# Optimization experiments

Hardware: AMD Instinct MI355X
Metric: run time of the kernel (lower is better)

The kernel has to match this reference:

```python
import jax, jax.numpy as jnp
import numpy as np

D_MODEL = 1024
N_HEADS = 16
ADAPTIVE_TEMP = 1.0
LN_EPS = 1e-5


def _sinusoidal_pe(max_len, d_model):
    pos = np.arange(max_len)[:, None].astype(np.float32)
    div = np.exp(np.arange(0, d_model, 2).astype(np.float32) * (-np.log(10000.0) / d_model))
    pe = np.zeros((max_len, d_model), dtype=np.float32)
    pe[:, 0::2] = np.sin(pos * div)
    pe[:, 1::2] = np.cos(pos * div)
    return jnp.asarray(pe)


def _mlp2(q, w1, b1, w2, b2):
    # Linear(1,h) -> ReLU -> Linear(h,d)
    return jax.nn.relu(q @ w1 + b1) @ w2 + b2


def setup_inputs() -> dict:
    key = jax.random.key(0)
    ks = jax.random.split(key, 24)
    B, T, D = 2, 2048, D_MODEL
    H2 = D // 2
    s = 0.02
    inp = {
        "x": jax.random.normal(ks[0], (B, T, D), jnp.float32),
        "quantile": jax.random.uniform(ks[1], (B, 1), jnp.float32),
        "quantile_importance": jax.random.uniform(ks[2], (100,), jnp.float32),
        "Wq": jax.random.normal(ks[3], (D, D), jnp.float32) * s,
        "bq": jnp.zeros((D,), jnp.float32),
        "Wk": jax.random.normal(ks[4], (D, D), jnp.float32) * s,
        "bk": jnp.zeros((D,), jnp.float32),
        "Wv": jax.random.normal(ks[5], (D, D), jnp.float32) * s,
        "bv": jnp.zeros((D,), jnp.float32),
        "Wo": jax.random.normal(ks[6], (D, D), jnp.float32) * s,
        "bo": jnp.zeros((D,), jnp.float32),
        "qpq_w1": jax.random.normal(ks[7], (1, H2), jnp.float32) * s,
        "qpq_b1": jnp.zeros((H2,), jnp.float32),
        "qpq_w2": jax.random.normal(ks[8], (H2, D), jnp.float32) * s,
        "qpq_b2": jnp.zeros((D,), jnp.float32),
        "qpk_w1": jax.random.normal(ks[9], (1, H2), jnp.float32) * s,
        "qpk_b1": jnp.zeros((H2,), jnp.float32),
        "qpk_w2": jax.random.normal(ks[10], (H2, D), jnp.float32) * s,
        "qpk_b2": jnp.zeros((D,), jnp.float32),
        "qpv_w1": jax.random.normal(ks[11], (1, H2), jnp.float32) * s,
        "qpv_b1": jnp.zeros((H2,), jnp.float32),
        "qpv_w2": jax.random.normal(ks[12], (H2, D), jnp.float32) * s,
        "qpv_b2": jnp.zeros((D,), jnp.float32),
        "ln_g": jnp.ones((D,), jnp.float32),
        "ln_b": jnp.zeros((D,), jnp.float32),
    }
    return inp


def reference(x, quantile, quantile_importance,
              Wq, bq, Wk, bk, Wv, bv, Wo, bo,
              qpq_w1, qpq_b1, qpq_w2, qpq_b2,
              qpk_w1, qpk_b1, qpk_w2, qpk_b2,
              qpv_w1, qpv_b1, qpv_w2, qpv_b2,
              ln_g, ln_b):
    B, T, D = x.shape
    H = N_HEADS
    dk = D // H

    # positional encoding
    x = x + _sinusoidal_pe(T, D)

    # quantile-conditioned embeddings [B, D]
    q_embed = _mlp2(quantile, qpq_w1, qpq_b1, qpq_w2, qpq_b2)
    k_embed = _mlp2(quantile, qpk_w1, qpk_b1, qpk_w2, qpk_b2)
    v_embed = _mlp2(quantile, qpv_w1, qpv_b1, qpv_w2, qpv_b2)

    # importance weight per batch (no-grad buffer lookup)
    buf = jax.lax.stop_gradient(quantile_importance)
    idx = jnp.clip((quantile[:, 0] * 100).astype(jnp.int32), 0, 99)
    mx = buf.max()
    imp = buf[idx]
    imp = jnp.where(mx > 0, imp / mx, imp)  # [B]

    Q = (x @ Wq + bq) + q_embed[:, None, :]
    K = (x @ Wk + bk) + k_embed[:, None, :]
    V = (x @ Wv + bv) + v_embed[:, None, :]

    # [B, H, T, dk]
    Q = Q.reshape(B, T, H, dk).transpose(0, 2, 1, 3)
    K = K.reshape(B, T, H, dk).transpose(0, 2, 1, 3)
    V = V.reshape(B, T, H, dk).transpose(0, 2, 1, 3)

    scores = jnp.einsum('bhtd,bhsd->bhts', Q, K) / jnp.sqrt(jnp.float32(dk))
    scale = 1.0 + imp * ADAPTIVE_TEMP  # [B]
    scores = scores * scale[:, None, None, None]

    attn = jax.nn.softmax(scores, axis=-1)  # dropout is identity at inference
    out = jnp.einsum('bhts,bhsd->bhtd', attn, V)
    out = out.transpose(0, 2, 1, 3).reshape(B, T, D)
    out = out @ Wo + bo

    y = x + out
    mu = y.mean(axis=-1, keepdims=True)
    var = y.var(axis=-1, keepdims=True)
    return (y - mu) / jnp.sqrt(var + LN_EPS) * ln_g + ln_b
```

## Files before the change

kernel.cpp:

```cpp
#include <hip/hip_runtime.h>

#define D 1024
#define T 2048
#define BATCH 2
#define NR 4096
#define NH 16
#define HID 512

typedef unsigned short u16;
typedef unsigned int u32;
typedef unsigned long long u64;
typedef float f32x4 __attribute__((ext_vector_type(4)));
typedef float f32x16 __attribute__((ext_vector_type(16)));
typedef __bf16 bf16x8 __attribute__((ext_vector_type(8)));

__device__ __forceinline__ u16 f2bf(float f) {
    union { __bf16 h; u16 u; } c; c.h = (__bf16)f; return c.u;
}

__device__ __forceinline__ u32 cvtpk(float a, float b) {
    u32 r;
    asm("v_cvt_pk_bf16_f32 %0, %1, %2" : "=v"(r) : "v"(a), "v"(b));
    return r;
}

__device__ __forceinline__ void plswap(u32& x, u32& y) {
    asm volatile("v_permlane32_swap_b32 %0, %1" : "+v"(x), "+v"(y));
}

__device__ __forceinline__ void gload16(const u16* g, u16* l) {
    __builtin_amdgcn_global_load_lds(
        (const __attribute__((address_space(1))) unsigned int*)g,
        (__attribute__((address_space(3))) unsigned int*)l,
        16, 0, 0);
}

__global__ __launch_bounds__(256) void k_mlp1(const float* __restrict__ qtl,
        const float* __restrict__ w1q, const float* __restrict__ b1q, const float* __restrict__ w2q,
        const float* __restrict__ w1k, const float* __restrict__ b1k, const float* __restrict__ w2k,
        const float* __restrict__ w1v, const float* __restrict__ b1v, const float* __restrict__ w2v,
        const float* __restrict__ qimp, float* __restrict__ part, float* __restrict__ scl)
{
    int dc = blockIdx.x;
    int jc = blockIdx.y;
    int wb = blockIdx.z;
    int which = wb >> 1, b = wb & 1;
    const float *w1, *b1, *w2;
    if (which == 0)      { w1 = w1q; b1 = b1q; w2 = w2q; }
    else if (which == 1) { w1 = w1k; b1 = b1k; w2 = w2k; }
    else                 { w1 = w1v; b1 = b1v; w2 = w2v; }
    int tid = threadIdx.x;
    __shared__ float h[128];
    if (tid < 128) {
        int j = jc * 128 + tid;
        h[tid] = fmaxf(qtl[b] * w1[j] + b1[j], 0.0f);
    }
    __syncthreads();
    int d = dc * 256 + tid;
    float acc = 0.0f;
    for (int j = 0; j < 128; ++j) acc += h[j] * w2[(size_t)(jc * 128 + j) * D + d];
    part[((size_t)wb * 4 + jc) * D + d] = acc;
    if (dc == 0 && jc == 0 && wb == 0 && tid < BATCH) {
        float mx = qimp[0];
        for (int i = 1; i < 100; ++i) mx = fmaxf(mx, qimp[i]);
        float q = qtl[tid];
        int idx = (int)(q * 100.0f);
        idx = idx < 0 ? 0 : (idx > 99 ? 99 : idx);
        float imp = qimp[idx];
        if (mx > 0.0f) imp /= mx;
        scl[tid] = 1.0f + imp;
    }
}

__global__ __launch_bounds__(256) void k_mlp2(const float* __restrict__ part,
        const float* __restrict__ b2q, const float* __restrict__ b2k, const float* __restrict__ b2v,
        float* __restrict__ embeds)
{
    int dc = blockIdx.x;
    int wb = blockIdx.y;
    int which = wb >> 1;
    const float* b2 = which == 0 ? b2q : which == 1 ? b2k : b2v;
    int d = dc * 256 + threadIdx.x;
    float acc = b2[d];
    #pragma unroll
    for (int jc = 0; jc < 4; ++jc) acc += part[((size_t)wb * 4 + jc) * D + d];
    embeds[(size_t)wb * D + d] = acc;
}

__global__ __launch_bounds__(256) void k_pe(const float* __restrict__ x,
                                            float* __restrict__ xpe, u16* __restrict__ xpeb)
{
    int idx = (blockIdx.x * 256 + threadIdx.x) * 4;
    int d = idx & (D - 1);
    int t = (idx >> 10) & (T - 1);
    const float KL = -0.0089944731946f;
    float ft = (float)t;
    float dv0 = __expf((float)d * KL);
    float dv1 = __expf((float)(d + 2) * KL);
    float a0 = ft * dv0, a1 = ft * dv1;
    float4 xv = *reinterpret_cast<const float4*>(x + idx);
    float4 r;
    r.x = xv.x + __sinf(a0);
    r.y = xv.y + __cosf(a0);
    r.z = xv.z + __sinf(a1);
    r.w = xv.w + __cosf(a1);
    *reinterpret_cast<float4*>(xpe + idx) = r;
    ushort4 o;
    o.x = f2bf(r.x); o.y = f2bf(r.y); o.z = f2bf(r.z); o.w = f2bf(r.w);
    *reinterpret_cast<ushort4*>(xpeb + idx) = o;
}

__global__ __launch_bounds__(256) void k_wconv(const float* __restrict__ Wq, const float* __restrict__ Wk,
                                               const float* __restrict__ Wv, const float* __restrict__ Wo,
                                               u16* __restrict__ Wt)
{
    __shared__ float tile[64][65];
    int z = blockIdx.z;
    const float* W = z == 0 ? Wq : z == 1 ? Wk : z == 2 ? Wv : Wo;
    u16* out = Wt + (size_t)z * D * D;
    int n0 = blockIdx.x * 64, k0 = blockIdx.y * 64;
    int r = threadIdx.x >> 4;
    int c4 = (threadIdx.x & 15) * 4;
    #pragma unroll
    for (int rr = 0; rr < 64; rr += 16) {
        float4 v = *reinterpret_cast<const float4*>(W + (size_t)(k0 + r + rr) * D + n0 + c4);
        tile[r + rr][c4 + 0] = v.x; tile[r + rr][c4 + 1] = v.y;
        tile[r + rr][c4 + 2] = v.z; tile[r + rr][c4 + 3] = v.w;
    }
    __syncthreads();
    #pragma unroll
    for (int rr = 0; rr < 64; rr += 16) {
        ushort4 o;
        o.x = f2bf(tile[c4 + 0][r + rr]);
        o.y = f2bf(tile[c4 + 1][r + rr]);
        o.z = f2bf(tile[c4 + 2][r + rr]);
        o.w = f2bf(tile[c4 + 3][r + rr]);
        *reinterpret_cast<ushort4*>(out + (size_t)(n0 + r + rr) * D + k0 + c4) = o;
    }
}

__device__ __forceinline__ void gemm128(const u16* __restrict__ Ag, const u16* __restrict__ Bg,
                                        int m0, int n0, f32x4 acc[4][4])
{
    __shared__ u16 As[128 * 64];
    __shared__ u16 Bs[128 * 64];
    const int tid = threadIdx.x;
    const int lane = tid & 63, wave = tid >> 6;
    const int wr = wave >> 1, wc = wave & 1;
    #pragma unroll
    for (int i = 0; i < 4; ++i)
        #pragma unroll
        for (int j = 0; j < 4; ++j)
            #pragma unroll
            for (int e = 0; e < 4; ++e) acc[i][j][e] = 0.0f;

    for (int kt = 0; kt < 16; ++kt) {
        __syncthreads();
        #pragma unroll
        for (int c = 0; c < 4; ++c) {
            int ci = c * 256 + tid;
            int row = ci >> 3;
            int sl = (ci & 7) ^ (row & 7);
            gload16(Ag + (size_t)(m0 + row) * D + kt * 64 + sl * 8, As + (size_t)ci * 8);
            gload16(Bg + (size_t)(n0 + row) * D + kt * 64 + sl * 8, Bs + (size_t)ci * 8);
        }
        __syncthreads();
        #pragma unroll
        for (int ks = 0; ks < 2; ++ks) {
            bf16x8 af[4], bfr[4];
            #pragma unroll
            for (int i = 0; i < 4; ++i) {
                int ra = wr * 64 + i * 16 + (lane & 15);
                int sa = ((ks * 4 + (lane >> 4)) ^ (ra & 7));
                af[i] = *reinterpret_cast<const bf16x8*>((const char*)As + ra * 128 + sa * 16);
                int rb = wc * 64 + i * 16 + (lane & 15);
                int sb = ((ks * 4 + (lane >> 4)) ^ (rb & 7));
                bfr[i] = *reinterpret_cast<const bf16x8*>((const char*)Bs + rb * 128 + sb * 16);
            }
            #pragma unroll
            for (int i = 0; i < 4; ++i)
                #pragma unroll
                for (int j = 0; j < 4; ++j)
                    acc[i][j] = __builtin_amdgcn_mfma_f32_16x16x32_bf16(af[i], bfr[j], acc[i][j], 0, 0, 0);
        }
    }
}

__global__ __launch_bounds__(256, 2)
void k_qkv(const u16* __restrict__ A, const u16* __restrict__ Wt,
           const float* __restrict__ bq, const float* __restrict__ bk, const float* __restrict__ bv,
           const float* __restrict__ embeds, const float* __restrict__ scl,
           u16* __restrict__ Qo, u16* __restrict__ Ko, u16* __restrict__ Vt)
{
    int which = blockIdx.z;
    const u16* Bg = Wt + (size_t)which * D * D;
    const float* bias = which == 0 ? bq : which == 1 ? bk : bv;
    const float* emb = embeds + which * (BATCH * D);
    int m0 = blockIdx.x * 128, n0 = blockIdx.y * 128;
    f32x4 acc[4][4];
    gemm128(A, Bg, m0, n0, acc);
    int lane = threadIdx.x & 63, wave = threadIdx.x >> 6;
    int wr = wave >> 1, wc = wave & 1;
    int rowbase = m0 + wr * 64 + ((lane >> 4) << 2);
    int colbase = n0 + wc * 64 + (lane & 15);
    if (which < 2) {
        u16* Out = which == 0 ? Qo : Ko;
        float sc0 = 1.0f, sc1 = 1.0f;
        if (which == 0) {
            sc0 = scl[0] * 0.125f * 1.44269504f;
            sc1 = scl[1] * 0.125f * 1.44269504f;
        }
        #pragma unroll
        for (int j = 0; j < 4; ++j) {
            int c = colbase + j * 16;
            float add0 = bias[c] + emb[c];
            float add1 = bias[c] + emb[D + c];
            #pragma unroll
            for (int i = 0; i < 4; ++i) {
                int rb = rowbase + i * 16;
                #pragma unroll
                for (int jj = 0; jj < 4; ++jj) {
                    int r = rb + jj;
                    float v = (r >> 11) ? (acc[i][j][jj] + add1) * sc1
                                        : (acc[i][j][jj] + add0) * sc0;
                    Out[(size_t)r * D + c] = f2bf(v);
                }
            }
        }
    } else {
        #pragma unroll
        for (int j = 0; j < 4; ++j) {
            int c = colbase + j * 16;
            int hh = c >> 6, cc = c & 63;
            float add0 = bias[c] + emb[c];
            float add1 = bias[c] + emb[D + c];
            #pragma unroll
            for (int i = 0; i < 4; ++i) {
                int rb = rowbase + i * 16;
                int bb = rb >> 11;
                int t = rb & (T - 1);
                float add = bb ? add1 : add0;
                ushort4 o;
                o.x = f2bf(acc[i][j][0] + add);
                o.y = f2bf(acc[i][j][1] + add);
                o.z = f2bf(acc[i][j][2] + add);
                o.w = f2bf(acc[i][j][3] + add);
                *reinterpret_cast<ushort4*>(Vt + ((size_t)((bb * NH + hh) * 64 + cc)) * T + t) = o;
            }
        }
    }
}

__global__ __launch_bounds__(256, 2)
void k_attn(const u16* __restrict__ Q, const u16* __restrict__ K, const u16* __restrict__ Vt,
            u16* __restrict__ AO)
{
    __shared__ u16 Ks[2][128 * 64];
    __shared__ u16 Vs[2][64 * 128];
    int bh = blockIdx.x;
    int b = bh >> 4, hh = bh & 15;
    int q0 = blockIdx.y * 128;
    int tid = threadIdx.x;
    int lane = tid & 63, w = tid >> 6;
    int q31 = lane & 31, h = lane >> 5;

    bf16x8 qf[4];
    {
        const u16* qp = Q + (size_t)(b * T + q0 + w * 32 + q31) * D + hh * 64 + h * 8;
        #pragma unroll
        for (int ds = 0; ds < 4; ++ds)
            qf[ds] = *reinterpret_cast<const bf16x8*>(qp + ds * 16);
    }

    f32x16 o0, o1;
    #pragma unroll
    for (int e = 0; e < 16; ++e) { o0[e] = 0.0f; o1[e] = 0.0f; }
    float m_run = -1e30f, l_run = 0.0f;

    #pragma unroll
    for (int c = 0; c < 4; ++c) {
        int ci = c * 256 + tid;
        int row = ci >> 3;
        int sl = (ci & 7) ^ (row & 7);
        gload16(K + (size_t)(b * T + row) * D + hh * 64 + sl * 8, Ks[0] + (size_t)ci * 8);
        int rv = ci >> 4;
        int sv = (ci & 15) ^ (rv & 7);
        gload16(Vt + (size_t)(bh * 64 + rv) * T + sv * 8, Vs[0] + (size_t)ci * 8);
    }
    __syncthreads();

    for (int kt = 0; kt < 16; ++kt) {
        int cur = kt & 1;
        if (kt < 15) {
            int t0 = (kt + 1) * 128;
            #pragma unroll
            for (int c = 0; c < 4; ++c) {
                int ci = c * 256 + tid;
                int row = ci >> 3;
                int sl = (ci & 7) ^ (row & 7);
                gload16(K + (size_t)(b * T + t0 + row) * D + hh * 64 + sl * 8, Ks[cur ^ 1] + (size_t)ci * 8);
                int rv = ci >> 4;
                int sv = (ci & 15) ^ (rv & 7);
                gload16(Vt + (size_t)(bh * 64 + rv) * T + t0 + sv * 8, Vs[cur ^ 1] + (size_t)ci * 8);
            }
        }
        const char* Ksc = (const char*)Ks[cur];
        const char* Vsc = (const char*)Vs[cur];

        f32x16 s[4];
        #pragma unroll
        for (int k2 = 0; k2 < 4; ++k2)
            #pragma unroll
            for (int e = 0; e < 16; ++e) s[k2][e] = 0.0f;
        __builtin_amdgcn_s_setprio(1);
        #pragma unroll
        for (int k2 = 0; k2 < 4; ++k2) {
            int rk = k2 * 32 + q31;
            int xm = rk & 7;
            #pragma unroll
            for (int ds = 0; ds < 4; ++ds) {
                int sp = (2 * ds + h) ^ xm;
                bf16x8 kf = *reinterpret_cast<const bf16x8*>(Ksc + rk * 128 + sp * 16);
                s[k2] = __builtin_amdgcn_mfma_f32_32x32x16_bf16(kf, qf[ds], s[k2], 0, 0, 0);
            }
        }
        __builtin_amdgcn_s_setprio(0);

        float mt = -1e30f;
        #pragma unroll
        for (int k2 = 0; k2 < 4; ++k2)
            #pragma unroll
            for (int e = 0; e < 16; ++e) mt = fmaxf(mt, s[k2][e]);
        mt = fmaxf(mt, __shfl_xor(mt, 32, 64));
        bool skip = __all((int)(mt <= m_run + 11.0f));
        if (!skip) {
            float mn = fmaxf(m_run, mt);
            float corr = __builtin_exp2f(m_run - mn);
            m_run = mn;
            l_run *= corr;
            #pragma unroll
            for (int reg = 0; reg < 16; ++reg) {
                int src = ((reg & 3) + 8 * (reg >> 2)) + ((lane & 32) >> 3);
                float cr = __shfl(corr, src, 64);
                o0[reg] *= cr;
                o1[reg] *= cr;
            }
        }
        float ps0 = 0.0f, ps1 = 0.0f;
        #pragma unroll
        for (int k2 = 0; k2 < 4; ++k2)
            #pragma unroll
            for (int e = 0; e < 16; ++e) {
                float p = __builtin_exp2f(s[k2][e] - m_run);
                s[k2][e] = p;
                if (k2 & 1) ps1 += p; else ps0 += p;
            }
        float psum = ps0 + ps1;
        psum += __shfl_xor(psum, 32, 64);
        l_run += psum;

        __builtin_amdgcn_s_setprio(1);
        #pragma unroll
        for (int k2 = 0; k2 < 4; ++k2) {
            u32 w0 = cvtpk(s[k2][0], s[k2][1]),   w1 = cvtpk(s[k2][2], s[k2][3]);
            u32 w2 = cvtpk(s[k2][4], s[k2][5]),   w3 = cvtpk(s[k2][6], s[k2][7]);
            u32 w4 = cvtpk(s[k2][8], s[k2][9]),   w5 = cvtpk(s[k2][10], s[k2][11]);
            u32 w6 = cvtpk(s[k2][12], s[k2][13]), w7 = cvtpk(s[k2][14], s[k2][15]);
            plswap(w0, w2); plswap(w1, w3);
            plswap(w4, w6); plswap(w5, w7);
            union { bf16x8 v; u32 u[4]; } plo, phi;
            plo.u[0] = w0; plo.u[1] = w1; plo.u[2] = w2; plo.u[3] = w3;
            phi.u[0] = w4; phi.u[1] = w5; phi.u[2] = w6; phi.u[3] = w7;
            int rv0 = q31, rv1 = 32 + q31;
            int x0 = rv0 & 7, x1 = rv1 & 7;
            int klo = 2 * k2, khi = 2 * k2 + 1;
            bf16x8 vf;
            vf = *reinterpret_cast<const bf16x8*>(Vsc + rv0 * 256 + (((2 * klo + h) ^ x0) << 4));
            o0 = __builtin_amdgcn_mfma_f32_32x32x16_bf16(plo.v, vf, o0, 0, 0, 0);
            vf = *reinterpret_cast<const bf16x8*>(Vsc + rv1 * 256 + (((2 * klo + h) ^ x1) << 4));
            o1 = __builtin_amdgcn_mfma_f32_32x32x16_bf16(plo.v, vf, o1, 0, 0, 0);
            vf = *reinterpret_cast<const bf16x8*>(Vsc + rv0 * 256 + (((2 * khi + h) ^ x0) << 4));
            o0 = __builtin_amdgcn_mfma_f32_32x32x16_bf16(phi.v, vf, o0, 0, 0, 0);
            vf = *reinterpret_cast<const bf16x8*>(Vsc + rv1 * 256 + (((2 * khi + h) ^ x1) << 4));
            o1 = __builtin_amdgcn_mfma_f32_32x32x16_bf16(phi.v, vf, o1, 0, 0, 0);
        }
        __builtin_amdgcn_s_setprio(0);
        __syncthreads();
    }

    float linv = 1.0f / l_run;
    #pragma unroll
    for (int reg = 0; reg < 16; ++reg) {
        int src = ((reg & 3) + 8 * (reg >> 2)) + ((lane & 32) >> 3);
        float li = __shfl(linv, src, 64);
        int qr = q0 + w * 32 + (reg & 3) + 8 * (reg >> 2) + 4 * h;
        size_t off = (size_t)(b * T + qr) * D + hh * 64 + q31;
        AO[off] = f2bf(o0[reg] * li);
        AO[off + 32] = f2bf(o1[reg] * li);
    }
}

__global__ __launch_bounds__(256, 2)
void k_ogemm(const u16* __restrict__ A, const u16* __restrict__ Wt,
             const float* __restrict__ bo, const float* __restrict__ xpe,
             float* __restrict__ y)
{
    int m0 = blockIdx.x * 128, n0 = blockIdx.y * 128;
    f32x4 acc[4][4];
    gemm128(A, Wt, m0, n0, acc);
    int lane = threadIdx.x & 63, wave = threadIdx.x >> 6;
    int wr = wave >> 1, wc = wave & 1;
    int rowbase = m0 + wr * 64 + ((lane >> 4) << 2);
    int colbase = n0 + wc * 64 + (lane & 15);
    #pragma unroll
    for (int j = 0; j < 4; ++j) {
        int c = colbase + j * 16;
        float bc = bo[c];
        #pragma unroll
        for (int i = 0; i < 4; ++i) {
            #pragma unroll
            for (int jj = 0; jj < 4; ++jj) {
                int r = rowbase + i * 16 + jj;
                y[(size_t)r * D + c] = acc[i][j][jj] + bc + xpe[(size_t)r * D + c];
            }
        }
    }
}

__global__ __launch_bounds__(256) void k_ln(const float* __restrict__ y, const float* __restrict__ g,
                                            const float* __restrict__ bb, float* __restrict__ out)
{
    int row = blockIdx.x;
    int tid = threadIdx.x;
    const float* yr = y + (size_t)row * D;
    float4 v = *reinterpret_cast<const float4*>(yr + tid * 4);
    float s = v.x + v.y + v.z + v.w;
    float s2 = v.x * v.x + v.y * v.y + v.z * v.z + v.w * v.w;
    #pragma unroll
    for (int off = 1; off < 64; off <<= 1) {
        s += __shfl_xor(s, off, 64);
        s2 += __shfl_xor(s2, off, 64);
    }
    __shared__ float red[8];
    int wave = tid >> 6, lane = tid & 63;
    if (lane == 0) { red[wave] = s; red[4 + wave] = s2; }
    __syncthreads();
    s = red[0] + red[1] + red[2] + red[3];
    s2 = red[4] + red[5] + red[6] + red[7];
    float mu = s * (1.0f / 1024.0f);
    float var = s2 * (1.0f / 1024.0f) - mu * mu;
    float rstd = rsqrtf(var + 1e-5f);
    float4 gv = *reinterpret_cast<const float4*>(g + tid * 4);
    float4 bv = *reinterpret_cast<const float4*>(bb + tid * 4);
    float4 o;
    o.x = (v.x - mu) * rstd * gv.x + bv.x;
    o.y = (v.y - mu) * rstd * gv.y + bv.y;
    o.z = (v.z - mu) * rstd * gv.z + bv.z;
    o.w = (v.w - mu) * rstd * gv.w + bv.w;
    *reinterpret_cast<float4*>(out + (size_t)row * D + tid * 4) = o;
}

extern "C" void kernel_launch(void* const* d_in, const int* in_sizes, int n_in,
                              void* d_out, int out_size, void* d_ws, size_t ws_size,
                              hipStream_t stream)
{
    const float* x    = (const float*)d_in[0];
    const float* qtl  = (const float*)d_in[1];
    const float* qimp = (const float*)d_in[2];
    const float* Wq = (const float*)d_in[3];
    const float* bq = (const float*)d_in[4];
    const float* Wk = (const float*)d_in[5];
    const float* bk = (const float*)d_in[6];
    const float* Wv = (const float*)d_in[7];
    const float* bv = (const float*)d_in[8];
    const float* Wo = (const float*)d_in[9];
    const float* bo = (const float*)d_in[10];
    const float* qpq_w1 = (const float*)d_in[11];
    const float* qpq_b1 = (const float*)d_in[12];
    const float* qpq_w2 = (const float*)d_in[13];
    const float* qpq_b2 = (const float*)d_in[14];
    const float* qpk_w1 = (const float*)d_in[15];
    const float* qpk_b1 = (const float*)d_in[16];
    const float* qpk_w2 = (const float*)d_in[17];
    const float* qpk_b2 = (const float*)d_in[18];
    const float* qpv_w1 = (const float*)d_in[19];
    const float* qpv_b1 = (const float*)d_in[20];
    const float* qpv_w2 = (const float*)d_in[21];
    const float* qpv_b2 = (const float*)d_in[22];
    const float* ln_g = (const float*)d_in[23];
    const float* ln_b = (const float*)d_in[24];
    (void)in_sizes; (void)n_in; (void)out_size; (void)ws_size;

    char* w = (char*)d_ws;
    float* xpe   = (float*)(w);
    u16* xpeb    = (u16*)(w + (16u << 20));
    u16* Wt      = (u16*)(w + (24u << 20));
    u16* Qb      = (u16*)(w + (32u << 20));
    u16* Kb      = (u16*)(w + (40u << 20));
    u16* Vtb     = (u16*)(w + (48u << 20));
    u16* AOb     = (u16*)(w + (56u << 20));
    float* yb    = (float*)(w + (32u << 20));
    float* emb   = (float*)(w + (64u << 20));
    float* scl   = (float*)(w + (64u << 20) + 32768);
    float* part  = (float*)(w + (64u << 20) + 65536);

    k_mlp1<<<dim3(4, 4, 6), 256, 0, stream>>>(qtl,
        qpq_w1, qpq_b1, qpq_w2,
        qpk_w1, qpk_b1, qpk_w2,
        qpv_w1, qpv_b1, qpv_w2,
        qimp, part, scl);
    k_mlp2<<<dim3(4, 6), 256, 0, stream>>>(part, qpq_b2, qpk_b2, qpv_b2, emb);
    k_pe<<<4096, 256, 0, stream>>>(x, xpe, xpeb);
    k_wconv<<<dim3(16, 16, 4), 256, 0, stream>>>(Wq, Wk, Wv, Wo, Wt);
    k_qkv<<<dim3(32, 8, 3), 256, 0, stream>>>(xpeb, Wt, bq, bk, bv, emb, scl, Qb, Kb, Vtb);
    k_attn<<<dim3(32, 16), 256, 0, stream>>>(Qb, Kb, Vtb, AOb);
    k_ogemm<<<dim3(32, 8), 256, 0, stream>>>(AOb, Wt + (size_t)3 * D * D, bo, xpe, yb);
    k_ln<<<4096, 256, 0, stream>>>(yb, ln_g, ln_b, (float*)d_out);
}
```

Before: 162.4 us.

## Split attention KV range across two wave groups per block with LDS merge

```diff
diff --git a/kernel.cpp b/kernel.cpp
--- a/kernel.cpp
+++ b/kernel.cpp
@@ -28,11 +28,30 @@
     asm volatile("v_permlane32_swap_b32 %0, %1" : "+v"(x), "+v"(y));
 }
 
+__device__ __forceinline__ float fmax3(float a, float b, float c) {
+    float r; asm("v_max3_f32 %0, %1, %2, %3" : "=v"(r) : "v"(a), "v"(b), "v"(c)); return r;
+}
+
+__device__ __forceinline__ float vmax16(const f32x16& v) {
+    float c0 = fmax3(v[0], v[1], v[2]);
+    float c1 = fmax3(v[3], v[4], v[5]);
+    float c2 = fmax3(v[6], v[7], v[8]);
+    float c3 = fmax3(v[9], v[10], v[11]);
+    c0 = fmax3(c0, v[12], v[13]);
+    c1 = fmax3(c1, v[14], v[15]);
+    c0 = fmax3(c0, c1, c2);
+    return fmaxf(c0, c3);
+}
+
 __device__ __forceinline__ void gload16(const u16* g, u16* l) {
     __builtin_amdgcn_global_load_lds(
         (const __attribute__((address_space(1))) unsigned int*)g,
         (__attribute__((address_space(3))) unsigned int*)l,
         16, 0, 0);
+}
+
+__device__ __forceinline__ int swz8(int row) {
+    return (row & 7) ^ ((row >> 3) & 3);
 }
 
 __global__ __launch_bounds__(256) void k_mlp1(const float* __restrict__ qtl,
@@ -251,22 +270,25 @@
     }
 }
 
-__global__ __launch_bounds__(256, 2)
+__global__ __launch_bounds__(512, 4)
 void k_attn(const u16* __restrict__ Q, const u16* __restrict__ K, const u16* __restrict__ Vt,
             u16* __restrict__ AO)
 {
-    __shared__ u16 Ks[2][128 * 64];
-    __shared__ u16 Vs[2][64 * 128];
+    __shared__ u16 Ks[2][2][64 * 64];
+    __shared__ u16 Vs[2][2][64 * 64];
     int bh = blockIdx.x;
     int b = bh >> 4, hh = bh & 15;
     int q0 = blockIdx.y * 128;
     int tid = threadIdx.x;
     int lane = tid & 63, w = tid >> 6;
+    int half = w >> 2, wq = w & 3;
     int q31 = lane & 31, h = lane >> 5;
+    int sh = tid >> 8, sti = tid & 255;
+    int kvb = sh * 1024;
 
     bf16x8 qf[4];
     {
-        const u16* qp = Q + (size_t)(b * T + q0 + w * 32 + q31) * D + hh * 64 + h * 8;
+        const u16* qp = Q + (size_t)(b * T + q0 + wq * 32 + q31) * D + hh * 64 + h * 8;
         #pragma unroll
         for (int ds = 0; ds < 4; ++ds)
             qf[ds] = *reinterpret_cast<const bf16x8*>(qp + ds * 16);
@@ -278,45 +300,41 @@
     float m_run = -1e30f, l_run = 0.0f;
 
     #pragma unroll
-    for (int c = 0; c < 4; ++c) {
-        int ci = c * 256 + tid;
+    for (int c = 0; c < 2; ++c) {
+        int ci = c * 256 + sti;
         int row = ci >> 3;
-        int sl = (ci & 7) ^ (row & 7);
-        gload16(K + (size_t)(b * T + row) * D + hh * 64 + sl * 8, Ks[0] + (size_t)ci * 8);
-        int rv = ci >> 4;
-        int sv = (ci & 15) ^ (rv & 7);
-        gload16(Vt + (size_t)(bh * 64 + rv) * T + sv * 8, Vs[0] + (size_t)ci * 8);
+        int sl = (ci & 7) ^ swz8(row);
+        gload16(K + (size_t)(b * T + kvb + row) * D + hh * 64 + sl * 8, Ks[sh][0] + (size_t)ci * 8);
+        gload16(Vt + (size_t)(bh * 64 + row) * T + kvb + sl * 8, Vs[sh][0] + (size_t)ci * 8);
     }
     __syncthreads();
 
     for (int kt = 0; kt < 16; ++kt) {
         int cur = kt & 1;
         if (kt < 15) {
-            int t0 = (kt + 1) * 128;
-            #pragma unroll
-            for (int c = 0; c < 4; ++c) {
-                int ci = c * 256 + tid;
+            int t0 = kvb + (kt + 1) * 64;
+            #pragma unroll
+            for (int c = 0; c < 2; ++c) {
+                int ci = c * 256 + sti;
                 int row = ci >> 3;
-                int sl = (ci & 7) ^ (row & 7);
-                gload16(K + (size_t)(b * T + t0 + row) * D + hh * 64 + sl * 8, Ks[cur ^ 1] + (size_t)ci * 8);
-                int rv = ci >> 4;
-                int sv = (ci & 15) ^ (rv & 7);
-                gload16(Vt + (size_t)(bh * 64 + rv) * T + t0 + sv * 8, Vs[cur ^ 1] + (size_t)ci * 8);
-            }
-        }
-        const char* Ksc = (const char*)Ks[cur];
-        const char* Vsc = (const char*)Vs[cur];
-
-        f32x16 s[4];
-        #pragma unroll
-        for (int k2 = 0; k2 < 4; ++k2)
+                int sl = (ci & 7) ^ swz8(row);
+                gload16(K + (size_t)(b * T + t0 + row) * D + hh * 64 + sl * 8, Ks[sh][cur ^ 1] + (size_t)ci * 8);
+                gload16(Vt + (size_t)(bh * 64 + row) * T + t0 + sl * 8, Vs[sh][cur ^ 1] + (size_t)ci * 8);
+            }
+        }
+        const char* Ksc = (const char*)Ks[half][cur];
+        const char* Vsc = (const char*)Vs[half][cur];
+
+        f32x16 s[2];
+        #pragma unroll
+        for (int k2 = 0; k2 < 2; ++k2)
             #pragma unroll
             for (int e = 0; e < 16; ++e) s[k2][e] = 0.0f;
         __builtin_amdgcn_s_setprio(1);
         #pragma unroll
-        for (int k2 = 0; k2 < 4; ++k2) {
+        for (int k2 = 0; k2 < 2; ++k2) {
             int rk = k2 * 32 + q31;
-            int xm = rk & 7;
+            int xm = swz8(rk);
             #pragma unroll
             for (int ds = 0; ds < 4; ++ds) {
                 int sp = (2 * ds + h) ^ xm;
@@ -326,11 +344,7 @@
         }
         __builtin_amdgcn_s_setprio(0);
 
-        float mt = -1e30f;
-        #pragma unroll
-        for (int k2 = 0; k2 < 4; ++k2)
-            #pragma unroll
-            for (int e = 0; e < 16; ++e) mt = fmaxf(mt, s[k2][e]);
+        float mt = fmaxf(vmax16(s[0]), vmax16(s[1]));
         mt = fmaxf(mt, __shfl_xor(mt, 32, 64));
         bool skip = __all((int)(mt <= m_run + 11.0f));
         if (!skip) {
@@ -346,22 +360,23 @@
                 o1[reg] *= cr;
             }
         }
-        float ps0 = 0.0f, ps1 = 0.0f;
-        #pragma unroll
-        for (int k2 = 0; k2 < 4; ++k2)
+        float ps0 = 0.0f, ps1 = 0.0f, ps2 = 0.0f, ps3 = 0.0f;
+        #pragma unroll
+        for (int k2 = 0; k2 < 2; ++k2)
             #pragma unroll
             for (int e = 0; e < 16; ++e) {
                 float p = __builtin_exp2f(s[k2][e] - m_run);
                 s[k2][e] = p;
-                if (k2 & 1) ps1 += p; else ps0 += p;
-            }
-        float psum = ps0 + ps1;
+                if ((e & 3) == 0) ps0 += p; else if ((e & 3) == 1) ps1 += p;
+                else if ((e & 3) == 2) ps2 += p; else ps3 += p;
+            }
+        float psum = (ps0 + ps1) + (ps2 + ps3);
         psum += __shfl_xor(psum, 32, 64);
         l_run += psum;
 
         __builtin_amdgcn_s_setprio(1);
         #pragma unroll
-        for (int k2 = 0; k2 < 4; ++k2) {
+        for (int k2 = 0; k2 < 2; ++k2) {
             u32 w0 = cvtpk(s[k2][0], s[k2][1]),   w1 = cvtpk(s[k2][2], s[k2][3]);
             u32 w2 = cvtpk(s[k2][4], s[k2][5]),   w3 = cvtpk(s[k2][6], s[k2][7]);
             u32 w4 = cvtpk(s[k2][8], s[k2][9]),   w5 = cvtpk(s[k2][10], s[k2][11]);
@@ -372,31 +387,58 @@
             plo.u[0] = w0; plo.u[1] = w1; plo.u[2] = w2; plo.u[3] = w3;
             phi.u[0] = w4; phi.u[1] = w5; phi.u[2] = w6; phi.u[3] = w7;
             int rv0 = q31, rv1 = 32 + q31;
-            int x0 = rv0 & 7, x1 = rv1 & 7;
+            int x0 = swz8(rv0), x1 = swz8(rv1);
             int klo = 2 * k2, khi = 2 * k2 + 1;
             bf16x8 vf;
-            vf = *reinterpret_cast<const bf16x8*>(Vsc + rv0 * 256 + (((2 * klo + h) ^ x0) << 4));
+            vf = *reinterpret_cast<const bf16x8*>(Vsc + rv0 * 128 + (((2 * klo + h) ^ x0) << 4));
             o0 = __builtin_amdgcn_mfma_f32_32x32x16_bf16(plo.v, vf, o0, 0, 0, 0);
-            vf = *reinterpret_cast<const bf16x8*>(Vsc + rv1 * 256 + (((2 * klo + h) ^ x1) << 4));
+            vf = *reinterpret_cast<const bf16x8*>(Vsc + rv1 * 128 + (((2 * klo + h) ^ x1) << 4));
             o1 = __builtin_amdgcn_mfma_f32_32x32x16_bf16(plo.v, vf, o1, 0, 0, 0);
-            vf = *reinterpret_cast<const bf16x8*>(Vsc + rv0 * 256 + (((2 * khi + h) ^ x0) << 4));
+            vf = *reinterpret_cast<const bf16x8*>(Vsc + rv0 * 128 + (((2 * khi + h) ^ x0) << 4));
             o0 = __builtin_amdgcn_mfma_f32_32x32x16_bf16(phi.v, vf, o0, 0, 0, 0);
-            vf = *reinterpret_cast<const bf16x8*>(Vsc + rv1 * 256 + (((2 * khi + h) ^ x1) << 4));
+            vf = *reinterpret_cast<const bf16x8*>(Vsc + rv1 * 128 + (((2 * khi + h) ^ x1) << 4));
             o1 = __builtin_amdgcn_mfma_f32_32x32x16_bf16(phi.v, vf, o1, 0, 0, 0);
         }
         __builtin_amdgcn_s_setprio(0);
         __syncthreads();
     }
 
-    float linv = 1.0f / l_run;
-    #pragma unroll
-    for (int reg = 0; reg < 16; ++reg) {
-        int src = ((reg & 3) + 8 * (reg >> 2)) + ((lane & 32) >> 3);
-        float li = __shfl(linv, src, 64);
-        int qr = q0 + w * 32 + (reg & 3) + 8 * (reg >> 2) + 4 * h;
-        size_t off = (size_t)(b * T + qr) * D + hh * 64 + q31;
-        AO[off] = f2bf(o0[reg] * li);
-        AO[off + 32] = f2bf(o1[reg] * li);
+    float* ML = (float*)Ks;
+    float* OB = (float*)Vs;
+    if (half == 1) {
+        if (h == 0) {
+            ML[(wq * 2 + 0) * 32 + q31] = m_run;
+            ML[(wq * 2 + 1) * 32 + q31] = l_run;
+        }
+        #pragma unroll
+        for (int reg = 0; reg < 16; ++reg) {
+            int row = (reg & 3) + 8 * (reg >> 2) + 4 * h;
+            OB[((size_t)wq * 32 + row) * 64 + q31] = o0[reg];
+            OB[((size_t)wq * 32 + row) * 64 + 32 + q31] = o1[reg];
+        }
+    }
+    __syncthreads();
+    if (half == 0) {
+        float mB = ML[(wq * 2 + 0) * 32 + q31];
+        float lB = ML[(wq * 2 + 1) * 32 + q31];
+        float mn = fmaxf(m_run, mB);
+        float ca = __builtin_exp2f(m_run - mn);
+        float cb = __builtin_exp2f(mB - mn);
+        float lf = ca * l_run + cb * lB;
+        float fa = ca / lf, fb = cb / lf;
+        #pragma unroll
+        for (int reg = 0; reg < 16; ++reg) {
+            int src = ((reg & 3) + 8 * (reg >> 2)) + ((lane & 32) >> 3);
+            float far = __shfl(fa, src, 64);
+            float fbr = __shfl(fb, src, 64);
+            int row = (reg & 3) + 8 * (reg >> 2) + 4 * h;
+            float b0 = OB[((size_t)wq * 32 + row) * 64 + q31];
+            float b1 = OB[((size_t)wq * 32 + row) * 64 + 32 + q31];
+            int qr = q0 + wq * 32 + row;
+            size_t off = (size_t)(b * T + qr) * D + hh * 64 + q31;
+            AO[off] = f2bf(o0[reg] * far + b0 * fbr);
+            AO[off + 32] = f2bf(o1[reg] * far + b1 * fbr);
+        }
     }
 }
 
@@ -513,7 +555,7 @@
     k_pe<<<4096, 256, 0, stream>>>(x, xpe, xpeb);
     k_wconv<<<dim3(16, 16, 4), 256, 0, stream>>>(Wq, Wk, Wv, Wo, Wt);
     k_qkv<<<dim3(32, 8, 3), 256, 0, stream>>>(xpeb, Wt, bq, bk, bv, emb, scl, Qb, Kb, Vtb);
-    k_attn<<<dim3(32, 16), 256, 0, stream>>>(Qb, Kb, Vtb, AOb);
+    k_attn<<<dim3(32, 16), 512, 0, stream>>>(Qb, Kb, Vtb, AOb);
     k_ogemm<<<dim3(32, 8), 256, 0, stream>>>(AOb, Wt + (size_t)3 * D * D, bo, xpe, yb);
     k_ln<<<4096, 256, 0, stream>>>(yb, ln_g, ln_b, (float*)d_out);
 }
```

Measured after the change: 159.9 us. Within noise of the previous version (-1.6%).
